# Kernel optimization log

Measured on AMD Instinct MI355X. Metric: run time of the kernel, lower is better.

Reference implementation:

```python
import jax, jax.numpy as jnp
import numpy as np

H = 4    # heads
D = 64   # embed_dim


def setup_inputs() -> dict:
    key = jax.random.key(0)
    ks = jax.random.split(key, 10)
    N, L = 128, 1024
    f = jnp.float32
    return {
        "seq_items": jax.random.normal(ks[0], (N, L, D), f),
        "target_items": jax.random.normal(ks[1], (N, D), f),
        "memory": jax.random.normal(ks[2], (N, D), f),
        # nn.Linear weights stored torch-style [out_features, in_features]
        "Wk": jax.random.normal(ks[3], (H * D, D), f) * 0.1,
        "Wq": jax.random.normal(ks[4], (H * D, D), f) * 0.1,
        "Wv": jax.random.normal(ks[5], (H * D, D), f) * 0.1,
        "Wu": jax.random.normal(ks[6], (D, H * D), f) * 0.1,
        "bu": jnp.zeros((D,), f),
        "W1": jax.random.normal(ks[7], (8, 4 * D), f) * 0.1,
        "b1": jnp.zeros((8,), f),
        "W2": jax.random.normal(ks[8], (1, 8), f) * 0.1,
        "b2": jnp.zeros((1,), f),
    }


def reference(seq_items, target_items, memory, Wk, Wq, Wv, Wu, bu, W1, b1, W2, b2):
    N, L, d = seq_items.shape
    # projections, split into heads: [N, L, H, D]
    e = (seq_items @ Wk.T).reshape(N, L, H, D)
    V = (seq_items @ Wv.T).reshape(N, L, H, D)
    v = (target_items @ Wq.T).reshape(N, 1, H, D)   # broadcast over L
    m = memory.reshape(N, 1, 1, D)                   # broadcast over L and heads
    # np.where(e_, 1, 0): 1 where nonzero
    mask = (e != 0).astype(e.dtype)
    a1 = (v - e) * mask
    a2 = (v * e) * mask
    a3 = (m - e) * mask
    a4 = (m * e) * mask
    alpha = jnp.concatenate([a1, a2, a3, a4], axis=-1)  # [N, L, H, 4D]
    # tiny MLP attention scorer: 4D -> 8 -> 1, sigmoid each
    hmid = jax.nn.sigmoid(alpha @ W1.T + b1)
    att = jax.nn.sigmoid(hmid @ W2.T + b2)              # [N, L, H, 1]
    out = jnp.einsum('nlhq,nlhd->nqhd', att, V).reshape(N, H * D)
    output = out @ Wu.T + bu                            # [N, D]
    return output, att
```

## Files before the change

kernel.cpp:

```cpp
#include <hip/hip_runtime.h>
#include <hip/hip_bf16.h>
#include <math.h>

#define NN 128
#define LL 1024
#define HH 4
#define DD 64
#define NCHUNK 8
#define CROWS 128

#define WS_ZT  0
#define WS_C   16384
#define WS_WTB 20480

typedef __attribute__((ext_vector_type(8))) short short8;
typedef __attribute__((ext_vector_type(4))) float f32x4;

__device__ __forceinline__ float sigm(float x) {
    return __builtin_amdgcn_rcpf(1.f + __expf(-x));
}

__device__ __forceinline__ short bf16s(float x) {
    __hip_bfloat16 h = __float2bfloat16(x);
    union { __hip_bfloat16 hh; short s; } u; u.hh = h;
    return u.s;
}

__device__ __forceinline__ short8 pack_bf8(float4 a, float4 b) {
    short8 r;
    r[0] = bf16s(a.x); r[1] = bf16s(a.y); r[2] = bf16s(a.z); r[3] = bf16s(a.w);
    r[4] = bf16s(b.x); r[5] = bf16s(b.y); r[6] = bf16s(b.z); r[7] = bf16s(b.w);
    return r;
}

__global__ void __launch_bounds__(256) precompute_kernel(
    const float* __restrict__ target, const float* __restrict__ memv,
    const float* __restrict__ Wk, const float* __restrict__ Wq,
    const float* __restrict__ Wv, const float* __restrict__ Wu,
    const float* __restrict__ W1, const float* __restrict__ b1,
    const float* __restrict__ bu,
    unsigned short* __restrict__ Wtb, float* __restrict__ cvg,
    float* __restrict__ Zt, float* __restrict__ out)
{
    const int b = blockIdx.x;
    const int t = threadIdx.x;

    if (b < 32) {
        const int idx = b * 256 + t;
        out[idx] = bu[idx & 63];
        return;
    }
    if (b < 96) {
        const int q = b - 32;
        const int h = t >> 6, k = t & 63;
        float s = 0.f;
        #pragma unroll 8
        for (int d = 0; d < 64; ++d)
            s = fmaf(Wu[q * 256 + h * 64 + d], Wv[(h * 64 + d) * 64 + k], s);
        Zt[t * 64 + q] = s;
        return;
    }

    const int nh = b - 96;
    const int n = nh >> 2, h = nh & 3;

    __shared__ __align__(16) float tl[64];
    __shared__ __align__(16) float ml[64];
    __shared__ float vh[64];
    __shared__ float wh[64 * 8];
    __shared__ float cp[64];
    __shared__ __align__(16) float wk_lds[64 * 64];

    if (t < 64)       tl[t] = target[n * 64 + t];
    else if (t < 128) ml[t - 64] = memv[n * 64 + (t - 64)];

    {
        const float4* src = reinterpret_cast<const float4*>(Wk + h * 4096);
        float4* dst = reinterpret_cast<float4*>(wk_lds);
        #pragma unroll
        for (int i = 0; i < 4; ++i)
            dst[i * 256 + t] = src[i * 256 + t];
    }
    __syncthreads();

    {
        const int d = t >> 2, kq = t & 3;
        const float4* wq4 = reinterpret_cast<const float4*>(Wq + (h * 64 + d) * 64 + kq * 16);
        const float4* tl4 = reinterpret_cast<const float4*>(tl + kq * 16);
        float s = 0.f;
        #pragma unroll
        for (int c = 0; c < 4; ++c) {
            const float4 a = wq4[c], bb = tl4[c];
            s = fmaf(a.x, bb.x, s); s = fmaf(a.y, bb.y, s);
            s = fmaf(a.z, bb.z, s); s = fmaf(a.w, bb.w, s);
        }
        s += __shfl_xor(s, 1);
        s += __shfl_xor(s, 2);
        if (kq == 0) vh[d] = s;
    }
    __syncthreads();

    {
        const int d = t & 63, jh = t >> 6;
        const float vv = vh[d], mm = ml[d];
        #pragma unroll
        for (int r = 0; r < 2; ++r) {
            const int j = jh + r * 4;
            float wv = -W1[j * 256 + d] - W1[j * 256 + 128 + d];
            wv = fmaf(W1[j * 256 + 64 + d], vv, wv);
            wv = fmaf(W1[j * 256 + 192 + d], mm, wv);
            wh[d * 8 + j] = wv;
        }
    }
    if (t < 64) {
        const int j = t >> 3, sl = t & 7;
        float s = 0.f;
        #pragma unroll
        for (int d8 = 0; d8 < 8; ++d8) {
            const int d = sl * 8 + d8;
            s = fmaf(W1[j * 256 + d], vh[d], s);
            s = fmaf(W1[j * 256 + 128 + d], ml[d], s);
        }
        cp[t] = s;
    }
    __syncthreads();
    if (t < 8) {
        float s = b1[t];
        #pragma unroll
        for (int sl = 0; sl < 8; ++sl) s += cp[t * 8 + sl];
        cvg[n * 32 + h * 8 + t] = s;
    }

    {
        const int k = t & 63, jp = t >> 6;
        float s0 = 0.f, s1 = 0.f;
        #pragma unroll 8
        for (int d = 0; d < 64; ++d) {
            const float wk = wk_lds[d * 64 + k];
            s0 = fmaf(wk, wh[d * 8 + jp], s0);
            s1 = fmaf(wk, wh[d * 8 + jp + 4], s1);
        }
        unsigned short* dst = Wtb + ((size_t)n * 32 + h * 8) * 64;
        dst[jp * 64 + k]       = (unsigned short)bf16s(s0);
        dst[(jp + 4) * 64 + k] = (unsigned short)bf16s(s1);
    }
}

__global__ void __launch_bounds__(256, 5) main_kernel(
    const float* __restrict__ seq, const unsigned short* __restrict__ Wtb,
    const float* __restrict__ cvg, const float* __restrict__ W2,
    const float* __restrict__ b2, const float* __restrict__ Zt,
    float* __restrict__ att_out, float* __restrict__ out)
{
    const int n = blockIdx.x >> 3;
    const int chunk = blockIdx.x & 7;
    const int l0 = chunk * CROWS;
    const int t = threadIdx.x;
    const int lane = t & 63;
    const int w = t >> 6;

    __shared__ __align__(16) short seq_bf[128 * 72];
    __shared__ __align__(16) short wt_lds[32 * 72];
    __shared__ float cvl[32];
    __shared__ __align__(16) float att_l[512];
    __shared__ __align__(16) float Tp_l[4][256];
    __shared__ float T_l[256];
    __shared__ float op[256];

    const float* sbase = seq + ((size_t)n * LL + l0) * 64;

    #pragma unroll
    for (int g = 0; g < 4; ++g) {
        const int p4 = g * 256 + t;
        const int l = p4 >> 3, seg = p4 & 7;
        const float* rp = sbase + l * 64 + seg * 8;
        const float4 a = *reinterpret_cast<const float4*>(rp);
        const float4 bb = *reinterpret_cast<const float4*>(rp + 4);
        *reinterpret_cast<short8*>(seq_bf + l * 72 + seg * 8) = pack_bf8(a, bb);
    }
    {
        const int row = t >> 3, seg = t & 7;
        const int4 wv = *reinterpret_cast<const int4*>(
            Wtb + ((size_t)n * 32 + row) * 64 + seg * 8);
        *reinterpret_cast<int4*>(wt_lds + row * 72 + seg * 8) = wv;
    }
    if (t < 32) cvl[t] = cvg[n * 32 + t];
    __syncthreads();

    const int rt = w & 1;
    const int ctbase = (w >> 1) * 4;
    const int g = lane >> 4;
    const int cidx = lane & 15;

    short8 afrag[2];
    #pragma unroll
    for (int ks = 0; ks < 2; ++ks)
        afrag[ks] = *reinterpret_cast<const short8*>(
            wt_lds + (rt * 16 + cidx) * 72 + ks * 32 + g * 8);

    f32x4 acc[4];
    #pragma unroll
    for (int ct = 0; ct < 4; ++ct)
        #pragma unroll
        for (int r = 0; r < 4; ++r)
            acc[ct][r] = cvl[rt * 16 + g * 4 + r];

    #pragma unroll
    for (int ct = 0; ct < 4; ++ct) {
        const int l = (ctbase + ct) * 16 + cidx;
        const short8 bf0 = *reinterpret_cast<const short8*>(seq_bf + l * 72 + g * 8);
        const short8 bf1 = *reinterpret_cast<const short8*>(seq_bf + l * 72 + 32 + g * 8);
        acc[ct] = __builtin_amdgcn_mfma_f32_16x16x32_bf16(afrag[0], bf0, acc[ct], 0, 0, 0);
        acc[ct] = __builtin_amdgcn_mfma_f32_16x16x32_bf16(afrag[1], bf1, acc[ct], 0, 0, 0);
    }

    {
        const float4 w2v = *reinterpret_cast<const float4*>(W2 + 4 * (g & 1));
        const float b2v = b2[0];
        #pragma unroll
        for (int ct = 0; ct < 4; ++ct) {
            float local = w2v.x * sigm(acc[ct][0]);
            local = fmaf(w2v.y, sigm(acc[ct][1]), local);
            local = fmaf(w2v.z, sigm(acc[ct][2]), local);
            local = fmaf(w2v.w, sigm(acc[ct][3]), local);
            local += __shfl_xor(local, 16);
            const float attv = sigm(b2v + local);
            if ((lane & 16) == 0) {
                const int l = (ctbase + ct) * 16 + cidx;
                const int h = 2 * rt + (g >> 1);
                att_l[l * 4 + h] = attv;
            }
        }
    }
    __syncthreads();

    {
        float* dst = att_out + ((size_t)n * LL + l0) * 4;
        dst[t] = att_l[t];
        dst[256 + t] = att_l[256 + t];
    }

    {
        float th0 = 0.f, th1 = 0.f, th2 = 0.f, th3 = 0.f;
        #pragma unroll 4
        for (int li = 0; li < 32; ++li) {
            const int l = w * 32 + li;
            const float s = __uint_as_float(
                ((unsigned)(unsigned short)seq_bf[l * 72 + lane]) << 16);
            const float4 a = *reinterpret_cast<const float4*>(att_l + l * 4);
            th0 = fmaf(a.x, s, th0); th1 = fmaf(a.y, s, th1);
            th2 = fmaf(a.z, s, th2); th3 = fmaf(a.w, s, th3);
        }
        Tp_l[w][0 * 64 + lane] = th0;
        Tp_l[w][1 * 64 + lane] = th1;
        Tp_l[w][2 * 64 + lane] = th2;
        Tp_l[w][3 * 64 + lane] = th3;
    }
    __syncthreads();

    T_l[t] = Tp_l[0][t] + Tp_l[1][t] + Tp_l[2][t] + Tp_l[3][t];
    __syncthreads();

    {
        const int q = t & 63, wq = t >> 6;
        float s = 0.f;
        #pragma unroll 8
        for (int i = 0; i < 64; ++i) {
            const int p = wq * 64 + i;
            s = fmaf(T_l[p], Zt[p * 64 + q], s);
        }
        op[t] = s;
    }
    __syncthreads();
    if (t < 64) {
        const float s = op[t] + op[64 + t] + op[128 + t] + op[192 + t];
        atomicAdd(out + n * 64 + t, s);
    }
}

extern "C" void kernel_launch(void* const* d_in, const int* in_sizes, int n_in,
                              void* d_out, int out_size, void* d_ws, size_t ws_size,
                              hipStream_t stream) {
    const float* seq    = (const float*)d_in[0];
    const float* target = (const float*)d_in[1];
    const float* memv   = (const float*)d_in[2];
    const float* Wk     = (const float*)d_in[3];
    const float* Wq     = (const float*)d_in[4];
    const float* Wv     = (const float*)d_in[5];
    const float* Wu     = (const float*)d_in[6];
    const float* bu     = (const float*)d_in[7];
    const float* W1     = (const float*)d_in[8];
    const float* b1     = (const float*)d_in[9];
    const float* W2     = (const float*)d_in[10];
    const float* b2     = (const float*)d_in[11];

    float* out = (float*)d_out;
    float* att = out + NN * DD;

    float* ws  = (float*)d_ws;
    float* Ztw = ws + WS_ZT;
    float* cvg = ws + WS_C;
    unsigned short* Wtb = (unsigned short*)(ws + WS_WTB);

    precompute_kernel<<<608, 256, 0, stream>>>(target, memv, Wk, Wq, Wv, Wu, W1, b1,
                                               bu, Wtb, cvg, Ztw, out);
    main_kernel<<<NN * NCHUNK, 256, 0, stream>>>(seq, Wtb, cvg, W2, b2, Ztw,
                                                 att, out);
}
```

Baseline: 21.86 us.

## Alias LDS buffers, raise occupancy, fold precompute side-work into per-head blocks

The main kernel's shared arrays are placed in one byte buffer with aliasing (Tp_l over wt_lds and seq tail, T_l over att_l), cutting LDS per block so the launch bound can rise from 5 to 6 blocks per SIMD. The weighted sequence reduction now reads two bf16 values per 32-bit LDS load and combines lane halves with a shuffle. The precompute kernel drops its 96 extra blocks by having the first 96 per-(n,h) blocks also do the Zt and bias-init work, shrinking the grid to 512. The aliasing depends on barrier ordering being correct, and the merged blocks in precompute take on extra serial work.

```diff
diff --git a/kernel.cpp b/kernel.cpp
--- a/kernel.cpp
+++ b/kernel.cpp
@@ -45,24 +45,20 @@
     const int b = blockIdx.x;
     const int t = threadIdx.x;
 
-    if (b < 32) {
-        const int idx = b * 256 + t;
-        out[idx] = bu[idx & 63];
-        return;
-    }
-    if (b < 96) {
-        const int q = b - 32;
-        const int h = t >> 6, k = t & 63;
+    if (b < 64) {
+        const int q = b;
+        const int h2 = t >> 6, k2 = t & 63;
         float s = 0.f;
         #pragma unroll 8
         for (int d = 0; d < 64; ++d)
-            s = fmaf(Wu[q * 256 + h * 64 + d], Wv[(h * 64 + d) * 64 + k], s);
+            s = fmaf(Wu[q * 256 + h2 * 64 + d], Wv[(h2 * 64 + d) * 64 + k2], s);
         Zt[t * 64 + q] = s;
-        return;
-    }
-
-    const int nh = b - 96;
-    const int n = nh >> 2, h = nh & 3;
+    } else if (b < 96) {
+        const int idx = (b - 64) * 256 + t;
+        out[idx] = bu[idx & 63];
+    }
+
+    const int n = b >> 2, h = b & 3;
 
     __shared__ __align__(16) float tl[64];
     __shared__ __align__(16) float ml[64];
@@ -146,7 +142,7 @@
     }
 }
 
-__global__ void __launch_bounds__(256, 5) main_kernel(
+__global__ void __launch_bounds__(256, 6) main_kernel(
     const float* __restrict__ seq, const unsigned short* __restrict__ Wtb,
     const float* __restrict__ cvg, const float* __restrict__ W2,
     const float* __restrict__ b2, const float* __restrict__ Zt,
@@ -159,13 +155,14 @@
     const int lane = t & 63;
     const int w = t >> 6;
 
-    __shared__ __align__(16) short seq_bf[128 * 72];
-    __shared__ __align__(16) short wt_lds[32 * 72];
-    __shared__ float cvl[32];
-    __shared__ __align__(16) float att_l[512];
-    __shared__ __align__(16) float Tp_l[4][256];
-    __shared__ float T_l[256];
-    __shared__ float op[256];
+    __shared__ __align__(16) char smem[25216];
+    short* seq_bf = reinterpret_cast<short*>(smem);
+    short* wt_lds = reinterpret_cast<short*>(smem + 18432);
+    float* Tp_l   = reinterpret_cast<float*>(smem + 18432);
+    float* cvl    = reinterpret_cast<float*>(smem + 23040);
+    float* att_l  = reinterpret_cast<float*>(smem + 23168);
+    float* T_l    = reinterpret_cast<float*>(smem + 23168);
+    float* op     = reinterpret_cast<float*>(smem + 24192);
 
     const float* sbase = seq + ((size_t)n * LL + l0) * 64;
 
@@ -241,24 +238,36 @@
     }
 
     {
-        float th0 = 0.f, th1 = 0.f, th2 = 0.f, th3 = 0.f;
+        const int kk = lane & 31;
+        const int lp = lane >> 5;
+        float t0h0 = 0.f, t0h1 = 0.f, t0h2 = 0.f, t0h3 = 0.f;
+        float t1h0 = 0.f, t1h1 = 0.f, t1h2 = 0.f, t1h3 = 0.f;
         #pragma unroll 4
-        for (int li = 0; li < 32; ++li) {
-            const int l = w * 32 + li;
-            const float s = __uint_as_float(
-                ((unsigned)(unsigned short)seq_bf[l * 72 + lane]) << 16);
+        for (int li = 0; li < 16; ++li) {
+            const int l = w * 32 + 2 * li + lp;
+            const unsigned u = reinterpret_cast<const unsigned*>(seq_bf + l * 72)[kk];
+            const float slo = __uint_as_float(u << 16);
+            const float shi = __uint_as_float(u & 0xFFFF0000u);
             const float4 a = *reinterpret_cast<const float4*>(att_l + l * 4);
-            th0 = fmaf(a.x, s, th0); th1 = fmaf(a.y, s, th1);
-            th2 = fmaf(a.z, s, th2); th3 = fmaf(a.w, s, th3);
-        }
-        Tp_l[w][0 * 64 + lane] = th0;
-        Tp_l[w][1 * 64 + lane] = th1;
-        Tp_l[w][2 * 64 + lane] = th2;
-        Tp_l[w][3 * 64 + lane] = th3;
-    }
-    __syncthreads();
-
-    T_l[t] = Tp_l[0][t] + Tp_l[1][t] + Tp_l[2][t] + Tp_l[3][t];
+            t0h0 = fmaf(a.x, slo, t0h0); t1h0 = fmaf(a.x, shi, t1h0);
+            t0h1 = fmaf(a.y, slo, t0h1); t1h1 = fmaf(a.y, shi, t1h1);
+            t0h2 = fmaf(a.z, slo, t0h2); t1h2 = fmaf(a.z, shi, t1h2);
+            t0h3 = fmaf(a.w, slo, t0h3); t1h3 = fmaf(a.w, shi, t1h3);
+        }
+        t0h0 += __shfl_xor(t0h0, 32); t1h0 += __shfl_xor(t1h0, 32);
+        t0h1 += __shfl_xor(t0h1, 32); t1h1 += __shfl_xor(t1h1, 32);
+        t0h2 += __shfl_xor(t0h2, 32); t1h2 += __shfl_xor(t1h2, 32);
+        t0h3 += __shfl_xor(t0h3, 32); t1h3 += __shfl_xor(t1h3, 32);
+        const int hb = lp * 2;
+        float2 wa, wb;
+        wa.x = lp ? t0h2 : t0h0;  wa.y = lp ? t1h2 : t1h0;
+        wb.x = lp ? t0h3 : t0h1;  wb.y = lp ? t1h3 : t1h1;
+        *reinterpret_cast<float2*>(Tp_l + w * 256 + (hb + 0) * 64 + 2 * kk) = wa;
+        *reinterpret_cast<float2*>(Tp_l + w * 256 + (hb + 1) * 64 + 2 * kk) = wb;
+    }
+    __syncthreads();
+
+    T_l[t] = Tp_l[0 * 256 + t] + Tp_l[1 * 256 + t] + Tp_l[2 * 256 + t] + Tp_l[3 * 256 + t];
     __syncthreads();
 
     {
@@ -302,7 +311,7 @@
     float* cvg = ws + WS_C;
     unsigned short* Wtb = (unsigned short*)(ws + WS_WTB);
 
-    precompute_kernel<<<608, 256, 0, stream>>>(target, memv, Wk, Wq, Wv, Wu, W1, b1,
+    precompute_kernel<<<512, 256, 0, stream>>>(target, memv, Wk, Wq, Wv, Wu, W1, b1,
                                                bu, Wtb, cvg, Ztw, out);
     main_kernel<<<NN * NCHUNK, 256, 0, stream>>>(seq, Wtb, cvg, W2, b2, Ztw,
                                                  att, out);
```

Result: slower. 23.16 us (+5.9%).
